# Kernel optimization log

Measured on AMD Instinct MI355X. Metric: run time of the kernel, lower is better.

Reference implementation:

```python
import jax, jax.numpy as jnp
import numpy as np

OBSERVE = 30

def setup_inputs() -> dict:
    key = jax.random.key(0)
    k1, k2, k3, k4 = jax.random.split(key, 4)
    B, T = 8192, 2048
    u = jax.random.normal(k1, (B, T, 1), dtype=jnp.float32)
    x0 = jax.random.normal(k2, (B, OBSERVE), dtype=jnp.float32)
    # scale weights small so the linear AR recurrence stays stable over T steps
    W_x = jax.random.normal(k3, (OBSERVE, 1), dtype=jnp.float32) * 0.05
    W_f = jax.random.normal(k4, (1, 1), dtype=jnp.float32)
    return {"u": u, "x0": x0, "W_x": W_x, "W_f": W_f}


def reference(u, x0, W_x, W_f):
    # u: [B, T, 1]; x0: [B, observe] initial shift-register state.
    # Per step (matching the Keras cell):
    #   out = x_set @ W_x + u_t @ W_f            -> [B, 1]
    #   x_set <- concat(x_set[:, 1:], out)        (shift register)
    def step(x_set, u_t):
        out = x_set @ W_x + u_t @ W_f            # [B, 1]
        x_new = jnp.concatenate([x_set[:, 1:], out], axis=1)
        return x_new, out

    u_tbf = jnp.swapaxes(u, 0, 1)                # [T, B, 1]
    _, outs = jax.lax.scan(step, x0, u_tbf)      # outs: [T, B, 1]
    return jnp.swapaxes(outs, 0, 1)              # [B, T, 1]
```

## Files before the change

### kernel.cpp

```cpp
#include <hip/hip_runtime.h>

#define NB   8192
#define NT   2048
#define OBS  30
#define LCH  32
#define CPH  32
#define HALF 1024
#define RPB  4
#define CSTR 36

__device__ __forceinline__ float step6(float (&r)[32], const float (&wx)[OBS],
                                       int j, float uwf) {
  float a0 = fmaf(wx[0], r[(j + 0) & 31], uwf);
  float a1 = wx[1] * r[(j + 1) & 31];
  float a2 = wx[2] * r[(j + 2) & 31];
  float a3 = wx[3] * r[(j + 3) & 31];
  float a4 = wx[4] * r[(j + 4) & 31];
  float a5 = wx[5] * r[(j + 5) & 31];
  #pragma unroll
  for (int i = 6; i < OBS; i += 6) {
    a0 = fmaf(wx[i],     r[(j + i)     & 31], a0);
    a1 = fmaf(wx[i + 1], r[(j + i + 1) & 31], a1);
    a2 = fmaf(wx[i + 2], r[(j + i + 2) & 31], a2);
    a3 = fmaf(wx[i + 3], r[(j + i + 3) & 31], a3);
    a4 = fmaf(wx[i + 4], r[(j + i + 4) & 31], a4);
    a5 = fmaf(wx[i + 5], r[(j + i + 5) & 31], a5);
  }
  float out = ((a0 + a1) + (a2 + a3)) + (a4 + a5);
  r[(j + 30) & 31] = out;
  return out;
}

__global__ void __launch_bounds__(128, 4)
k_fused(const float* __restrict__ u, const float* __restrict__ x0,
        const float* __restrict__ Wx, const float* __restrict__ Wf,
        float* __restrict__ out) {
  __shared__ float tile[RPB * CPH * CSTR];
  __shared__ float sbuf[RPB * 32];
  const int tid  = threadIdx.x;
  const int g    = tid >> 5, k = tid & 31;
  const int row0 = blockIdx.x * RPB;

  float wx[OBS];
  #pragma unroll
  for (int i = 0; i < OBS; ++i) wx[i] = Wx[i];
  const float wf = Wf[0];

  float4 stg[8];
  const float* ub = u + (size_t)row0 * NT;
  #pragma unroll
  for (int i = 0; i < 8; ++i) {
    int v = i * 128 + tid, rr = v >> 8, p = v & 255;
    stg[i] = *(const float4*)(ub + (size_t)rr * NT + 4 * p);
  }

  {
    float r[32];
    #pragma unroll
    for (int i = 0; i < 32; ++i) r[i] = (k < OBS && i == k) ? 1.f : 0.f;
    #pragma unroll
    for (int j = 0; j < 32; ++j) {
      float o = step6(r, wx, j, 0.f);
      if (tid < 32) tile[j * 33 + k] = o;
    }
  }
  __syncthreads();
  float c0[OBS];
  #pragma unroll
  for (int i = 0; i < OBS; ++i) c0[i] = tile[k * 33 + i];
  if (k < OBS) sbuf[g * 32 + k] = x0[(size_t)(row0 + g) * OBS + k];
  __syncthreads();

  float* sl = &sbuf[g * 32];

  #pragma unroll 1
  for (int h = 0; h < 2; ++h) {
    #pragma unroll
    for (int i = 0; i < 8; ++i) {
      int v = i * 128 + tid, rr = v >> 8, p = v & 255;
      int c = p >> 3, t = 4 * (p & 7);
      *(float4*)(&tile[(rr * CPH + c) * CSTR + t]) = stg[i];
    }
    __syncthreads();

    {
      float r[32];
      #pragma unroll
      for (int i = 0; i < 32; ++i) r[i] = 0.f;
      float* tc = &tile[(g * CPH + k) * CSTR];
      #pragma unroll
      for (int q = 0; q < 8; ++q) {
        float4 u4 = *(const float4*)(tc + 4 * q);
        float4 o4;
        o4.x = step6(r, wx, 4 * q + 0, wf * u4.x);
        o4.y = step6(r, wx, 4 * q + 1, wf * u4.y);
        o4.z = step6(r, wx, 4 * q + 2, wf * u4.z);
        o4.w = step6(r, wx, 4 * q + 3, wf * u4.w);
        *(float4*)(tc + 4 * q) = o4;
      }
    }

    if (h == 0) {
      #pragma unroll
      for (int i = 0; i < 8; ++i) {
        int v = i * 128 + tid, rr = v >> 8, p = v & 255;
        stg[i] = *(const float4*)(ub + (size_t)rr * NT + HALF + 4 * p);
      }
    }
    __builtin_amdgcn_wave_barrier();

    float* ob = out + (size_t)(row0 + g) * NT + h * HALF;
    const float* tg = &tile[g * CPH * CSTR];
    #pragma unroll 1
    for (int c = 0; c < CPH; ++c) {
      float sv[32];
      #pragma unroll
      for (int q = 0; q < 8; ++q) {
        float4 v = *(const float4*)(sl + 4 * q);
        sv[4 * q] = v.x; sv[4 * q + 1] = v.y;
        sv[4 * q + 2] = v.z; sv[4 * q + 3] = v.w;
      }
      float p0 = tg[c * CSTR + k];
      float a0 = fmaf(c0[0], sv[0], p0);
      float a1 = c0[1] * sv[1];
      float a2 = c0[2] * sv[2];
      float a3 = c0[3] * sv[3];
      #pragma unroll
      for (int i = 4; i < 28; i += 4) {
        a0 = fmaf(c0[i],     sv[i],     a0);
        a1 = fmaf(c0[i + 1], sv[i + 1], a1);
        a2 = fmaf(c0[i + 2], sv[i + 2], a2);
        a3 = fmaf(c0[i + 3], sv[i + 3], a3);
      }
      a0 = fmaf(c0[28], sv[28], a0);
      a1 = fmaf(c0[29], sv[29], a1);
      float t0 = (a0 + a1) + (a2 + a3);
      if (k >= 2) sl[k - 2] = t0;
      ob[c * 32 + k] = t0;
      __builtin_amdgcn_wave_barrier();
    }
    __syncthreads();
  }
}

extern "C" void kernel_launch(void* const* d_in, const int* in_sizes, int n_in,
                              void* d_out, int out_size, void* d_ws, size_t ws_size,
                              hipStream_t stream) {
  const float* u  = (const float*)d_in[0];
  const float* x0 = (const float*)d_in[1];
  const float* Wx = (const float*)d_in[2];
  const float* Wf = (const float*)d_in[3];
  float* out = (float*)d_out;

  hipLaunchKernelGGL(k_fused, dim3(NB / RPB), dim3(128), 0, stream,
                     u, x0, Wx, Wf, out);
}
```

Baseline: 54.57 us.

## Use 64-step chunks with wave64 readlane state carry instead of LDS

Chunk length doubles from 32 to 64 steps. One thread now owns a whole 64-step chunk, and one 64-lane wave walks 32 chunks sequentially per row. The row state carried between chunks is broadcast with readlane from the previous chunk's last 30 outputs, replacing LDS round-trips and wave barriers. The whole row's u is loaded at once rather than double-buffered in halves. This removes the LDS shared-state traffic and halves the number of serial combine steps per row, at the cost of larger staging registers, lower occupancy (launch bounds 2) and no overlap of loads with compute.

Result: slower. 87.49 us (+60.3%).

```diff
diff --git a/kernel.cpp b/kernel.cpp
--- a/kernel.cpp
+++ b/kernel.cpp
@@ -3,11 +3,11 @@
 #define NB   8192
 #define NT   2048
 #define OBS  30
-#define LCH  32
-#define CPH  32
-#define HALF 1024
+#define LCH  64
+#define CCH  32
 #define RPB  4
-#define CSTR 36
+#define NTHR 128
+#define CSTR 68
 
 __device__ __forceinline__ float step6(float (&r)[32], const float (&wx)[OBS],
                                        int j, float uwf) {
@@ -31,14 +31,18 @@
   return out;
 }
 
-__global__ void __launch_bounds__(128, 4)
+__device__ __forceinline__ float rl(float v, int lane) {
+  return __uint_as_float(__builtin_amdgcn_readlane(__float_as_uint(v), lane));
+}
+
+__global__ void __launch_bounds__(NTHR, 2)
 k_fused(const float* __restrict__ u, const float* __restrict__ x0,
         const float* __restrict__ Wx, const float* __restrict__ Wf,
         float* __restrict__ out) {
-  __shared__ float tile[RPB * CPH * CSTR];
-  __shared__ float sbuf[RPB * 32];
+  __shared__ float tile[RPB * CCH * CSTR];
   const int tid  = threadIdx.x;
-  const int g    = tid >> 5, k = tid & 31;
+  const int wv   = tid >> 6;
+  const int k    = tid & 63;
   const int row0 = blockIdx.x * RPB;
 
   float wx[OBS];
@@ -46,100 +50,90 @@
   for (int i = 0; i < OBS; ++i) wx[i] = Wx[i];
   const float wf = Wf[0];
 
-  float4 stg[8];
+  float4 stg[16];
   const float* ub = u + (size_t)row0 * NT;
   #pragma unroll
-  for (int i = 0; i < 8; ++i) {
-    int v = i * 128 + tid, rr = v >> 8, p = v & 255;
+  for (int i = 0; i < 16; ++i) {
+    int v = i * NTHR + tid, rr = v >> 9, p = v & 511;
     stg[i] = *(const float4*)(ub + (size_t)rr * NT + 4 * p);
   }
 
-  {
+  if (tid < 32) {
     float r[32];
     #pragma unroll
-    for (int i = 0; i < 32; ++i) r[i] = (k < OBS && i == k) ? 1.f : 0.f;
+    for (int i = 0; i < 32; ++i) r[i] = (tid < OBS && i == tid) ? 1.f : 0.f;
     #pragma unroll
-    for (int j = 0; j < 32; ++j) {
-      float o = step6(r, wx, j, 0.f);
-      if (tid < 32) tile[j * 33 + k] = o;
-    }
+    for (int q = 0; q < 16; ++q)
+      #pragma unroll
+      for (int e = 0; e < 4; ++e) {
+        float o = step6(r, wx, (4 * q + e) & 31, 0.f);
+        if (tid < OBS) tile[(4 * q + e) * 33 + tid] = o;
+      }
   }
   __syncthreads();
   float c0[OBS];
   #pragma unroll
   for (int i = 0; i < OBS; ++i) c0[i] = tile[k * 33 + i];
-  if (k < OBS) sbuf[g * 32 + k] = x0[(size_t)(row0 + g) * OBS + k];
   __syncthreads();
 
-  float* sl = &sbuf[g * 32];
+  #pragma unroll
+  for (int i = 0; i < 16; ++i) {
+    int v = i * NTHR + tid, rr = v >> 9, p = v & 511;
+    int c = p >> 4, q = p & 15;
+    *(float4*)(&tile[(rr * CCH + c) * CSTR + 4 * q]) = stg[i];
+  }
+  __syncthreads();
+
+  {
+    float r[32];
+    #pragma unroll
+    for (int i = 0; i < 32; ++i) r[i] = 0.f;
+    float* tc = &tile[tid * CSTR];
+    #pragma unroll
+    for (int q = 0; q < 16; ++q) {
+      float4 u4 = *(const float4*)(tc + 4 * q);
+      float4 o4;
+      o4.x = step6(r, wx, (4 * q + 0) & 31, wf * u4.x);
+      o4.y = step6(r, wx, (4 * q + 1) & 31, wf * u4.y);
+      o4.z = step6(r, wx, (4 * q + 2) & 31, wf * u4.z);
+      o4.w = step6(r, wx, (4 * q + 3) & 31, wf * u4.w);
+      *(float4*)(tc + 4 * q) = o4;
+    }
+  }
+  __syncthreads();
 
   #pragma unroll 1
-  for (int h = 0; h < 2; ++h) {
-    #pragma unroll
-    for (int i = 0; i < 8; ++i) {
-      int v = i * 128 + tid, rr = v >> 8, p = v & 255;
-      int c = p >> 3, t = 4 * (p & 7);
-      *(float4*)(&tile[(rr * CPH + c) * CSTR + t]) = stg[i];
-    }
-    __syncthreads();
-
-    {
-      float r[32];
+  for (int rr2 = 0; rr2 < 2; ++rr2) {
+    const int lr  = wv * 2 + rr2;
+    const int row = row0 + lr;
+    float vprev = (k >= 34) ? x0[(size_t)row * OBS + (k - 34)] : 0.f;
+    const float* trow = &tile[lr * CCH * CSTR];
+    float* orow = out + (size_t)row * NT;
+    #pragma unroll 1
+    for (int c = 0; c < CCH; ++c) {
+      float sv[OBS];
       #pragma unroll
-      for (int i = 0; i < 32; ++i) r[i] = 0.f;
-      float* tc = &tile[(g * CPH + k) * CSTR];
-      #pragma unroll
-      for (int q = 0; q < 8; ++q) {
-        float4 u4 = *(const float4*)(tc + 4 * q);
-        float4 o4;
-        o4.x = step6(r, wx, 4 * q + 0, wf * u4.x);
-        o4.y = step6(r, wx, 4 * q + 1, wf * u4.y);
-        o4.z = step6(r, wx, 4 * q + 2, wf * u4.z);
-        o4.w = step6(r, wx, 4 * q + 3, wf * u4.w);
-        *(float4*)(tc + 4 * q) = o4;
-      }
-    }
-
-    if (h == 0) {
-      #pragma unroll
-      for (int i = 0; i < 8; ++i) {
-        int v = i * 128 + tid, rr = v >> 8, p = v & 255;
-        stg[i] = *(const float4*)(ub + (size_t)rr * NT + HALF + 4 * p);
-      }
-    }
-    __builtin_amdgcn_wave_barrier();
-
-    float* ob = out + (size_t)(row0 + g) * NT + h * HALF;
-    const float* tg = &tile[g * CPH * CSTR];
-    #pragma unroll 1
-    for (int c = 0; c < CPH; ++c) {
-      float sv[32];
-      #pragma unroll
-      for (int q = 0; q < 8; ++q) {
-        float4 v = *(const float4*)(sl + 4 * q);
-        sv[4 * q] = v.x; sv[4 * q + 1] = v.y;
-        sv[4 * q + 2] = v.z; sv[4 * q + 3] = v.w;
-      }
-      float p0 = tg[c * CSTR + k];
-      float a0 = fmaf(c0[0], sv[0], p0);
+      for (int i = 0; i < OBS; ++i) sv[i] = rl(vprev, 34 + i);
+      float p = trow[c * CSTR + k];
+      float a0 = fmaf(c0[0], sv[0], p);
       float a1 = c0[1] * sv[1];
       float a2 = c0[2] * sv[2];
       float a3 = c0[3] * sv[3];
+      float a4 = c0[4] * sv[4];
+      float a5 = c0[5] * sv[5];
       #pragma unroll
-      for (int i = 4; i < 28; i += 4) {
+      for (int i = 6; i < OBS; i += 6) {
         a0 = fmaf(c0[i],     sv[i],     a0);
         a1 = fmaf(c0[i + 1], sv[i + 1], a1);
         a2 = fmaf(c0[i + 2], sv[i + 2], a2);
         a3 = fmaf(c0[i + 3], sv[i + 3], a3);
+        a4 = fmaf(c0[i + 4], sv[i + 4], a4);
+        a5 = fmaf(c0[i + 5], sv[i + 5], a5);
       }
-      a0 = fmaf(c0[28], sv[28], a0);
-      a1 = fmaf(c0[29], sv[29], a1);
-      float t0 = (a0 + a1) + (a2 + a3);
-      if (k >= 2) sl[k - 2] = t0;
-      ob[c * 32 + k] = t0;
-      __builtin_amdgcn_wave_barrier();
+      float t0 = ((a0 + a1) + (a2 + a3)) + (a4 + a5);
+      orow[c * 64 + k] = t0;
+      vprev = t0;
     }
-    __syncthreads();
   }
 }
 
@@ -152,6 +146,6 @@
   const float* Wf = (const float*)d_in[3];
   float* out = (float*)d_out;
 
-  hipLaunchKernelGGL(k_fused, dim3(NB / RPB), dim3(128), 0, stream,
+  hipLaunchKernelGGL(k_fused, dim3(NB / RPB), dim3(NTHR), 0, stream,
                      u, x0, Wx, Wf, out);
 }
```
